# Performance work log

Measured on AMD Instinct MI355X. Metric: run time of the kernel, lower is better.

## Reference

```python
import jax, jax.numpy as jnp
import numpy as np

NUM_HEADS = 16
HEAD_DIM = 64  # hidden = 1024


def setup_inputs() -> dict:
    key = jax.random.key(0)
    k1, k2, k3 = jax.random.split(key, 3)
    B, S, Hd = 4, 4096, NUM_HEADS * HEAD_DIM
    x = jax.random.normal(k1, (B, S, Hd), dtype=jnp.float32)
    # xavier-uniform-ish scaling for the dense kernels
    Wqkv = jax.random.normal(k2, (Hd, 3 * Hd), dtype=jnp.float32) * (2.0 / (Hd + 3 * Hd)) ** 0.5
    bqkv = jnp.zeros((3 * Hd,), dtype=jnp.float32)
    Wout = jax.random.normal(k3, (Hd, Hd), dtype=jnp.float32) * (1.0 / Hd) ** 0.5
    bout = jnp.zeros((Hd,), dtype=jnp.float32)
    return {"x": x, "Wqkv": Wqkv, "bqkv": bqkv, "Wout": Wout, "bout": bout}


def reference(x, Wqkv, bqkv, Wout, bout):
    B, S, _ = x.shape
    H, D = NUM_HEADS, HEAD_DIM
    qkv = jnp.einsum('bsc,cf->bsf', x, Wqkv) + bqkv  # [B,S,3*H*D]
    q, k, v = jnp.split(qkv, 3, axis=-1)
    # source transposes to [B,H,S,D] before calling flax dot_product_attention_weights,
    # which interprets dims as [..., q_len=H, num_heads=S, depth=D]  (shape bug, kept faithfully)
    q = q.reshape(B, S, H, D).transpose(0, 2, 1, 3)  # [B,H,S,D]
    k = k.reshape(B, S, H, D).transpose(0, 2, 1, 3)
    v = v.reshape(B, S, H, D).transpose(0, 2, 1, 3)
    scale = D ** -0.5
    # flax: einsum('...qhd,...khd->...hqk') -> weights [B, S, H, H]
    logits = jnp.einsum('bqhd,bkhd->bhqk', q * scale, k)
    attn = jax.nn.softmax(logits, axis=-1)  # softmax over key-head axis
    # source: einsum('bhqk,bkhd->bqhd', weights, v) -> [B, H, S, D]
    out = jnp.einsum('bhqk,bkhd->bqhd', attn, v)
    out = out.transpose(0, 2, 1, 3).reshape(B, S, H * D)  # [B,S,hidden]
    return jnp.einsum('bsc,cf->bsf', out, Wout) + bout
```

## Files before the change

kernel.cpp:

```cpp
#include <hip/hip_runtime.h>
#include <hip/hip_bf16.h>

using bf16 = __hip_bfloat16;
typedef __bf16 bf16x8_t __attribute__((ext_vector_type(8)));
typedef float f32x4_t __attribute__((ext_vector_type(4)));

__device__ __forceinline__ void gl16(bf16* l, const bf16* g) {
  __builtin_amdgcn_global_load_lds(
      (const __attribute__((address_space(1))) unsigned int*)g,
      (__attribute__((address_space(3))) unsigned int*)l, 16, 0, 0);
}

#define BARRIER() do { asm volatile("" ::: "memory"); __builtin_amdgcn_s_barrier(); asm volatile("" ::: "memory"); } while (0)
#define WAITVM(N) asm volatile("s_waitcnt vmcnt(" #N ")" ::: "memory")

__global__ __launch_bounds__(256) void cvt_f32_bf16(const float* __restrict__ in,
                                                    bf16* __restrict__ out, int n4) {
  int i = blockIdx.x * 256 + threadIdx.x;
  if (i >= n4) return;
  float4 v = ((const float4*)in)[i];
  union { ushort4 u; bf16 b[4]; } o;
  o.b[0] = __float2bfloat16(v.x);
  o.b[1] = __float2bfloat16(v.y);
  o.b[2] = __float2bfloat16(v.z);
  o.b[3] = __float2bfloat16(v.w);
  ((ushort4*)out)[i] = o.u;
}

__global__ __launch_bounds__(256) void transpose_cvt(const float* __restrict__ in,
                                                     bf16* __restrict__ out, int R, int C) {
  __shared__ float t[32][33];
  int bx = blockIdx.x * 32, by = blockIdx.y * 32;
  int tx = threadIdx.x & 31, ty = threadIdx.x >> 5;
#pragma unroll
  for (int r = 0; r < 32; r += 8)
    t[ty + r][tx] = in[(size_t)(by + ty + r) * C + bx + tx];
  __syncthreads();
#pragma unroll
  for (int r = 0; r < 32; r += 8)
    out[(size_t)(bx + ty + r) * R + by + tx] = __float2bfloat16(t[tx][ty + r]);
}


template <int MH, int NH>
__device__ __forceinline__ void phase_loads(const bf16* lb, int wr, int wc, int lr, int lg, int exr,
                                            bf16x8_t (&af)[4][2], bf16x8_t (&bfr)[2][2]) {
  const bf16* ab = lb + MH * 8192;
  const bf16* bb = lb + (2 + NH) * 8192;
#pragma unroll
  for (int mi = 0; mi < 4; ++mi) {
    int R = wr * 64 + mi * 16 + lr;
    af[mi][0] = *(const bf16x8_t*)(ab + R * 64 + ((lg * 8) ^ exr));
    af[mi][1] = *(const bf16x8_t*)(ab + R * 64 + ((32 + lg * 8) ^ exr));
  }
#pragma unroll
  for (int ni = 0; ni < 2; ++ni) {
    int R = wc * 32 + ni * 16 + lr;
    bfr[ni][0] = *(const bf16x8_t*)(bb + R * 64 + ((lg * 8) ^ exr));
    bfr[ni][1] = *(const bf16x8_t*)(bb + R * 64 + ((32 + lg * 8) ^ exr));
  }
}

template <int MH, int NH>
__device__ __forceinline__ void phase_mfma(bf16x8_t (&af)[4][2], bf16x8_t (&bfr)[2][2],
                                           f32x4_t (&acc)[8][4]) {
  __builtin_amdgcn_s_setprio(1);
#pragma unroll
  for (int mi = 0; mi < 4; ++mi)
#pragma unroll
    for (int ni = 0; ni < 2; ++ni) {
      f32x4_t& a = acc[MH * 4 + mi][NH * 2 + ni];
      a = __builtin_amdgcn_mfma_f32_16x16x32_bf16(af[mi][0], bfr[ni][0], a, 0, 0, 0);
      a = __builtin_amdgcn_mfma_f32_16x16x32_bf16(af[mi][1], bfr[ni][1], a, 0, 0, 0);
    }
  __builtin_amdgcn_s_setprio(0);
}

#define DO_PHASE(BUF, MH, NH, STAGE, WAIT) do {                          \
    bf16x8_t af[4][2], bfr[2][2];                                        \
    phase_loads<MH, NH>(lds + (BUF) * 32768, wr, wc, lr, lg, exr, af, bfr); \
    STAGE; WAIT;                                                         \
    BARRIER();                                                           \
    phase_mfma<MH, NH>(af, bfr, acc);                                    \
    BARRIER();                                                           \
  } while (0)

template <int OUT_BF16, int NWGX>
__global__ __launch_bounds__(512, 2) void gemm256p(const bf16* __restrict__ A,
                                                   const bf16* __restrict__ Bt,
                                                   const float* __restrict__ bias,
                                                   void* __restrict__ Cv) {
  constexpr int K = 1024;
  constexpr int N = NWGX * 256;
  constexpr int TT = NWGX / 4;
  constexpr int G = TT * 16;
  constexpr int CPX = NWGX * 8;

  __shared__ __align__(16) bf16 lds[65536];
  const int tid = threadIdx.x;
  const int bx = blockIdx.x;

  const int wid = tid >> 6, lane = tid & 63;
  const int wr = wid >> 2, wc = wid & 3;
  const int lr = lane & 15, lg = lane >> 4;
  const int exr = (lr & 7) << 3;

  const int srow = tid >> 3;
  const int colg = ((((tid & 7) * 16) ^ ((srow & 7) << 4)) >> 1);
  const int browc0 = (srow >> 5) * 64 + (srow & 31);

  auto tileMN = [&](int tt, int& m0, int& n0) {
    int orig = bx + (tt << 8);
    int swz = (orig & 7) * CPX + (orig >> 3);
    m0 = (swz / NWGX) * 256;
    n0 = (swz % NWGX) * 256;
  };

  auto stageA = [&](int g, int h) {
    if (g >= G) return;
    int m0, n0; tileMN(g >> 4, m0, n0);
    const bf16* g0 = A + (size_t)(m0 + h * 64 + srow) * K + (g & 15) * 64 + colg;
    bf16* l = lds + (g & 1) * 32768 + h * 8192 + tid * 8;
    gl16(l, g0); gl16(l + 4096, g0 + (size_t)128 * K);
  };
  auto stageB = [&](int g, int h) {
    if (g >= G) return;
    int m0, n0; tileMN(g >> 4, m0, n0);
    const bf16* g0 = Bt + (size_t)(n0 + browc0 + h * 32) * K + (g & 15) * 64 + colg;
    bf16* l = lds + (g & 1) * 32768 + (2 + h) * 8192 + tid * 8;
    gl16(l, g0); gl16(l + 4096, g0 + (size_t)128 * K);
  };

  f32x4_t acc[8][4] = {};

  stageA(0, 0); stageB(0, 0); stageA(0, 1); stageB(0, 1);
  stageA(1, 0); stageB(1, 0);
  WAITVM(4);
  BARRIER();

  for (int g = 0; g < G; ++g) {
    const int buf = g & 1;
    DO_PHASE(buf, 0, 0, stageA(g + 1, 1), (void)0);
    DO_PHASE(buf, 0, 1, stageB(g + 1, 1), (void)0);
    DO_PHASE(buf, 1, 0, stageA(g + 2, 0), (void)0);
    if (g < G - 2) {
      DO_PHASE(buf, 1, 1, stageB(g + 2, 0), WAITVM(4));
    } else if (g == G - 2) {
      DO_PHASE(buf, 1, 1, (void)0, WAITVM(0));
    } else {
      DO_PHASE(buf, 1, 1, (void)0, (void)0);
    }

    if ((g & 15) == 15) {
      int m0, n0; tileMN(g >> 4, m0, n0);
#pragma unroll
      for (int m = 0; m < 8; ++m) {
        int row = m0 + wr * 128 + m * 16 + lg * 4;
#pragma unroll
        for (int j = 0; j < 4; ++j) {
#pragma unroll
          for (int n = 0; n < 4; ++n) {
            int col = n0 + wc * 64 + n * 16 + lr;
            float v = acc[m][n][j] + bias[col];
            if (OUT_BF16)
              ((bf16*)Cv)[(size_t)(row + j) * N + col] = __float2bfloat16(v);
            else
              ((float*)Cv)[(size_t)(row + j) * N + col] = v;
            acc[m][n][j] = 0.f;
          }
        }
      }
    }
  }
}

#define PSTR 48
__global__ __launch_bounds__(256) void attn_tok(const bf16* __restrict__ qkv,
                                                bf16* __restrict__ out) {
  __shared__ __align__(16) bf16 vs[4][1024];
  __shared__ __align__(16) bf16 ps[4][16 * PSTR];
  const int w = threadIdx.x >> 6, l = threadIdx.x & 63;
  const int t = blockIdx.x * 4 + w;
  const int lr = l & 15, lg = l >> 4;
  const bf16* base = qkv + (size_t)t * 3072;

  bf16x8_t v0 = *(const bf16x8_t*)(base + 2048 + l * 16);
  bf16x8_t v1 = *(const bf16x8_t*)(base + 2048 + l * 16 + 8);
  *(bf16x8_t*)(&vs[w][l * 16]) = v0;
  *(bf16x8_t*)(&vs[w][l * 16 + 8]) = v1;

  *(unsigned long long*)(&ps[w][(l >> 2) * PSTR + 16 + (l & 3) * 4]) = 0ULL;

  const bf16* qp = base + lr * 64 + lg * 8;
  const bf16* kp = base + 1024 + lr * 64 + lg * 8;
  bf16x8_t qa0 = *(const bf16x8_t*)qp;
  bf16x8_t ka0 = *(const bf16x8_t*)kp;
  bf16x8_t qa1 = *(const bf16x8_t*)(qp + 32);
  bf16x8_t ka1 = *(const bf16x8_t*)(kp + 32);
  f32x4_t s = {};
  s = __builtin_amdgcn_mfma_f32_16x16x32_bf16(qa0, ka0, s, 0, 0, 0);
  s = __builtin_amdgcn_mfma_f32_16x16x32_bf16(qa1, ka1, s, 0, 0, 0);

#pragma unroll
  for (int j = 0; j < 4; ++j) {
    float x = s[j] * 0.125f;
    float mx = x;
#pragma unroll
    for (int off = 8; off; off >>= 1) mx = fmaxf(mx, __shfl_xor(mx, off, 16));
    float e = __expf(x - mx);
    float sum = e;
#pragma unroll
    for (int off = 8; off; off >>= 1) sum += __shfl_xor(sum, off, 16);
    ps[w][(lg * 4 + j) * PSTR + lr] = __float2bfloat16(e / sum);
  }

  bf16x8_t pf = *(const bf16x8_t*)(&ps[w][lr * PSTR + lg * 8]);
  bf16x8_t vf[4] = {};
  if (l < 32) {
#pragma unroll
    for (int c = 0; c < 4; ++c)
#pragma unroll
      for (int j = 0; j < 8; ++j)
        vf[c][j] = (__bf16)vs[w][(lg * 8 + j) * 64 + c * 16 + lr];
  }
  f32x4_t o[4] = {};
#pragma unroll
  for (int c = 0; c < 4; ++c)
    o[c] = __builtin_amdgcn_mfma_f32_16x16x32_bf16(pf, vf[c], o[c], 0, 0, 0);

  bf16* ob = out + (size_t)t * 1024;
#pragma unroll
  for (int c = 0; c < 4; ++c)
#pragma unroll
    for (int j = 0; j < 4; ++j)
      ob[(lg * 4 + j) * 64 + c * 16 + lr] = __float2bfloat16(o[c][j]);
}

extern "C" void kernel_launch(void* const* d_in, const int* in_sizes, int n_in,
                              void* d_out, int out_size, void* d_ws, size_t ws_size,
                              hipStream_t stream) {
  const float* x    = (const float*)d_in[0];
  const float* Wqkv = (const float*)d_in[1];
  const float* bqkv = (const float*)d_in[2];
  const float* Wout = (const float*)d_in[3];
  const float* bout = (const float*)d_in[4];
  float* y = (float*)d_out;

  const int T = 16384, HD = 1024, N1 = 3072;

  char* ws = (char*)d_ws;
  size_t off = 0;
  bf16* xb  = (bf16*)(ws + off); off += (size_t)T * HD * 2;
  bf16* w1t = (bf16*)(ws + off); off += (size_t)N1 * HD * 2;
  bf16* w2t = (bf16*)(ws + off); off += (size_t)HD * HD * 2;
  bf16* qkv = (bf16*)(ws + off); off += (size_t)T * N1 * 2;
  if (ws_size < off) return;
  bf16* ao = xb;

  cvt_f32_bf16<<<(T * HD / 4 + 255) / 256, 256, 0, stream>>>(x, xb, T * HD / 4);
  transpose_cvt<<<dim3(N1 / 32, HD / 32), 256, 0, stream>>>(Wqkv, w1t, HD, N1);
  transpose_cvt<<<dim3(HD / 32, HD / 32), 256, 0, stream>>>(Wout, w2t, HD, HD);

  gemm256p<1, 12><<<256, 512, 0, stream>>>(xb, w1t, bqkv, qkv);
  attn_tok<<<T / 4, 256, 0, stream>>>(qkv, ao);
  gemm256p<0, 4><<<256, 512, 0, stream>>>(ao, w2t, bout, y);
}
```

Baseline: 219.5 us.

## Software-pipeline LDS fragment reads against MFMA phases in GEMM main loop

```diff
diff --git a/kernel.cpp b/kernel.cpp
--- a/kernel.cpp
+++ b/kernel.cpp
@@ -13,6 +13,7 @@
 
 #define BARRIER() do { asm volatile("" ::: "memory"); __builtin_amdgcn_s_barrier(); asm volatile("" ::: "memory"); } while (0)
 #define WAITVM(N) asm volatile("s_waitcnt vmcnt(" #N ")" ::: "memory")
+#define SCHED0() __builtin_amdgcn_sched_barrier(0)
 
 __global__ __launch_bounds__(256) void cvt_f32_bf16(const float* __restrict__ in,
                                                     bf16* __restrict__ out, int n4) {
@@ -42,17 +43,19 @@
 }
 
 
-template <int MH, int NH>
-__device__ __forceinline__ void phase_loads(const bf16* lb, int wr, int wc, int lr, int lg, int exr,
-                                            bf16x8_t (&af)[4][2], bf16x8_t (&bfr)[2][2]) {
-  const bf16* ab = lb + MH * 8192;
-  const bf16* bb = lb + (2 + NH) * 8192;
+__device__ __forceinline__ void readA(const bf16* lb, int half, int wr, int lr, int lg, int exr,
+                                      bf16x8_t (&af)[4][2]) {
+  const bf16* ab = lb + half * 8192;
 #pragma unroll
   for (int mi = 0; mi < 4; ++mi) {
     int R = wr * 64 + mi * 16 + lr;
     af[mi][0] = *(const bf16x8_t*)(ab + R * 64 + ((lg * 8) ^ exr));
     af[mi][1] = *(const bf16x8_t*)(ab + R * 64 + ((32 + lg * 8) ^ exr));
   }
+}
+__device__ __forceinline__ void readB(const bf16* lb, int half, int wc, int lr, int lg, int exr,
+                                      bf16x8_t (&bfr)[2][2]) {
+  const bf16* bb = lb + (2 + half) * 8192;
 #pragma unroll
   for (int ni = 0; ni < 2; ++ni) {
     int R = wc * 32 + ni * 16 + lr;
@@ -62,8 +65,8 @@
 }
 
 template <int MH, int NH>
-__device__ __forceinline__ void phase_mfma(bf16x8_t (&af)[4][2], bf16x8_t (&bfr)[2][2],
-                                           f32x4_t (&acc)[8][4]) {
+__device__ __forceinline__ void mfma16(bf16x8_t (&af)[4][2], bf16x8_t (&bfr)[2][2],
+                                       f32x4_t (&acc)[8][4]) {
   __builtin_amdgcn_s_setprio(1);
 #pragma unroll
   for (int mi = 0; mi < 4; ++mi)
@@ -75,15 +78,6 @@
     }
   __builtin_amdgcn_s_setprio(0);
 }
-
-#define DO_PHASE(BUF, MH, NH, STAGE, WAIT) do {                          \
-    bf16x8_t af[4][2], bfr[2][2];                                        \
-    phase_loads<MH, NH>(lds + (BUF) * 32768, wr, wc, lr, lg, exr, af, bfr); \
-    STAGE; WAIT;                                                         \
-    BARRIER();                                                           \
-    phase_mfma<MH, NH>(af, bfr, acc);                                    \
-    BARRIER();                                                           \
-  } while (0)
 
 template <int OUT_BF16, int NWGX>
 __global__ __launch_bounds__(512, 2) void gemm256p(const bf16* __restrict__ A,
@@ -132,27 +126,52 @@
   };
 
   f32x4_t acc[8][4] = {};
+  bf16x8_t af1[4][2], af2[4][2], b0[2][2], b1[2][2];
 
   stageA(0, 0); stageB(0, 0); stageA(0, 1); stageB(0, 1);
   stageA(1, 0); stageB(1, 0);
   WAITVM(4);
   BARRIER();
+  readA(lds, 0, wr, lr, lg, exr, af1);
+  readB(lds, 0, wc, lr, lg, exr, b0);
 
   for (int g = 0; g < G; ++g) {
-    const int buf = g & 1;
-    DO_PHASE(buf, 0, 0, stageA(g + 1, 1), (void)0);
-    DO_PHASE(buf, 0, 1, stageB(g + 1, 1), (void)0);
-    DO_PHASE(buf, 1, 0, stageA(g + 2, 0), (void)0);
-    if (g < G - 2) {
-      DO_PHASE(buf, 1, 1, stageB(g + 2, 0), WAITVM(4));
-    } else if (g == G - 2) {
-      DO_PHASE(buf, 1, 1, (void)0, WAITVM(0));
-    } else {
-      DO_PHASE(buf, 1, 1, (void)0, (void)0);
-    }
+    const bf16* cb = lds + (g & 1) * 32768;
+    const bf16* nb = lds + ((g & 1) ^ 1) * 32768;
+
+    stageA(g + 1, 1);
+    BARRIER();
+    readB(cb, 1, wc, lr, lg, exr, b1);
+    SCHED0();
+    mfma16<0, 0>(af1, b0, acc);
+    BARRIER();
+
+    stageB(g + 1, 1);
+    BARRIER();
+    readA(cb, 1, wr, lr, lg, exr, af2);
+    SCHED0();
+    mfma16<0, 1>(af1, b1, acc);
+    BARRIER();
+
+    stageA(g + 2, 0);
+    BARRIER();
+    mfma16<1, 0>(af2, b0, acc);
+    BARRIER();
+
+    stageB(g + 2, 0);
+    if (g < G - 2) { WAITVM(4); } else { WAITVM(0); }
+    BARRIER();
+    readA(nb, 0, wr, lr, lg, exr, af1);
+    readB(nb, 0, wc, lr, lg, exr, b0);
+    SCHED0();
+    mfma16<1, 1>(af2, b1, acc);
+    BARRIER();
 
     if ((g & 15) == 15) {
       int m0, n0; tileMN(g >> 4, m0, n0);
+      float bv[4];
+#pragma unroll
+      for (int n = 0; n < 4; ++n) bv[n] = bias[n0 + wc * 64 + n * 16 + lr];
 #pragma unroll
       for (int m = 0; m < 8; ++m) {
         int row = m0 + wr * 128 + m * 16 + lg * 4;
@@ -161,7 +180,7 @@
 #pragma unroll
           for (int n = 0; n < 4; ++n) {
             int col = n0 + wc * 64 + n * 16 + lr;
-            float v = acc[m][n][j] + bias[col];
+            float v = acc[m][n][j] + bv[n];
             if (OUT_BF16)
               ((bf16*)Cv)[(size_t)(row + j) * N + col] = __float2bfloat16(v);
             else
```

Result: faster. 207.6 us (-5.4%).
